# Performance work log

Measured on AMD Instinct MI355X. Metric: run time of the kernel, lower is better.

## Reference

```python
import jax, jax.numpy as jnp
import numpy as np

N = 100000
E = 1600000
F_IN = 256
F_OUT = 128
ALPHA = 0.2  # leaky relu slope


def setup_inputs() -> dict:
    key = jax.random.key(0)
    ks = jax.random.split(key, 8)
    x = jax.random.normal(ks[0], (N, F_IN), dtype=jnp.float32)
    edge_index = jax.random.randint(ks[1], (2, E), 0, N, dtype=jnp.int64)
    edge_attr = jax.random.normal(ks[2], (E,), dtype=jnp.float32)
    # xavier-normal-ish params
    weight = jax.random.normal(ks[3], (F_IN, F_OUT), dtype=jnp.float32) * (1.414 * np.sqrt(2.0 / (F_IN + F_OUT)))
    bias = jnp.zeros((F_OUT,), dtype=jnp.float32)
    a_l = jax.random.normal(ks[4], (F_OUT,), dtype=jnp.float32) * 0.1
    a_r = jax.random.normal(ks[5], (F_OUT,), dtype=jnp.float32) * 0.1
    fc = jax.random.normal(ks[6], (F_OUT, 1), dtype=jnp.float32) * (1.414 * np.sqrt(2.0 / (F_OUT + 1)))
    bf = jnp.zeros((1,), dtype=jnp.float32)
    return {"x": x, "edge_index": edge_index, "edge_attr": edge_attr,
            "weight": weight, "bias": bias, "a_l": a_l, "a_r": a_r,
            "fc": fc, "bf": bf}


def _segment_softmax(val, seg, num_segments):
    # numerically stable softmax over edges grouped by destination row
    seg_max = jax.ops.segment_max(val, seg, num_segments=num_segments)
    val = jnp.exp(val - seg_max[seg])
    seg_sum = jax.ops.segment_sum(val, seg, num_segments=num_segments)
    return val / (seg_sum[seg] + 1e-16)


def reference(x, edge_index, edge_attr, weight, bias, a_l, a_r, fc, bf):
    # dropout layers are identity in eval mode (deterministic reference)
    h = x @ weight                                   # [N, F_OUT]
    row, col = edge_index[0], edge_index[1]          # dst, src
    # GAT-style edge attention: leaky_relu(a_l.h[dst] + a_r.h[src])
    score_l = h @ a_l                                # [N]
    score_r = h @ a_r                                # [N]
    e = score_l[row] + score_r[col]                  # [E]
    e = jnp.where(e > 0, e, ALPHA * e)
    # row-softmax normalization over incoming edges of each dst node
    val = _segment_softmax(e, row, N)                # [E]
    # spmm: out[i] = sum_{(i,j) in E} val_ij * h[j]
    val_h = jax.ops.segment_sum(val[:, None] * h[col], row, num_segments=N)  # [N, F_OUT]
    val_h = jnp.where(jnp.isnan(val_h), 0.0, val_h)
    val_h = val_h + bias
    # NodeAdaptiveEncoder: relu(x) + sigmoid(x@fc + bf) * min(x, 0)
    gate = jax.nn.sigmoid(val_h @ fc + bf)           # [N, 1]
    out = jnp.where(val_h < 0, 0.0, val_h) + gate * jnp.where(val_h > 0, 0.0, val_h)
    return out
```

## Files before the change

### kernel.cpp

```cpp
#include <hip/hip_runtime.h>

#define N_NODES 100000
#define N_EDGES 1600000
#define FIN 256
#define FOUT 128
#define LRELU_ALPHA 0.2f
#define LOG2E 1.4426950408889634f

#define NBUCKET 391
#define PBLOCKS 256
#define PCHUNK  (N_EDGES / PBLOCKS)
#define BCAP    5120

using bf16x8 = __attribute__((ext_vector_type(8))) short;
using f32x4  = __attribute__((ext_vector_type(4))) float;

static __device__ __forceinline__ unsigned short f2bf(float f) {
    union { float f; unsigned u; } v; v.f = f;
    unsigned r = (v.u + 0x7FFF + ((v.u >> 16) & 1)) >> 16;
    return (unsigned short)r;
}

static __device__ __forceinline__ bf16x8 cvt8(float4 a, float4 b) {
    union { bf16x8 v; unsigned short u[8]; } r;
    r.u[0] = f2bf(a.x); r.u[1] = f2bf(a.y); r.u[2] = f2bf(a.z); r.u[3] = f2bf(a.w);
    r.u[4] = f2bf(b.x); r.u[5] = f2bf(b.y); r.u[6] = f2bf(b.z); r.u[7] = f2bf(b.w);
    return r.v;
}

static __device__ __forceinline__ void gld_lds16(const unsigned short* g, unsigned short* l) {
    __builtin_amdgcn_global_load_lds(
        (const __attribute__((address_space(1))) unsigned int*)g,
        (__attribute__((address_space(3))) unsigned int*)l, 16, 0, 0);
}

static __device__ __forceinline__ void acc8(float* acc, uint4 r, float w) {
    union { uint4 u; _Float16 h[8]; } c; c.u = r;
#pragma unroll
    for (int k = 0; k < 8; ++k)
        acc[k] = fmaf((float)c.h[k], w, acc[k]);
}

static __device__ __forceinline__ float edgew(float sl, float sr) {
    float e = sl + sr;
    return exp2f(fmaf(fminf(e, 0.f), LRELU_ALPHA, fmaxf(e, 0.f)));
}

__global__ void k_wt(const float* __restrict__ w, unsigned short* __restrict__ wt_sw,
                     int* __restrict__ bcnt)
{
    if (blockIdx.x == 0)
        for (int z = threadIdx.x; z < NBUCKET; z += 256) bcnt[z] = 0;
    int i = blockIdx.x * blockDim.x + threadIdx.x;
    if (i >= FIN * FOUT) return;
    int k = i >> 7, n = i & 127;
    wt_sw[n * FIN + (((k >> 3) ^ (n & 7)) << 3) + (k & 7)] = f2bf(w[k * FOUT + n]);
}

__global__ __launch_bounds__(256, 2) void k_gemm3(
    const float* __restrict__ x, const unsigned short* __restrict__ wt_sw,
    const float* __restrict__ a_l, const float* __restrict__ a_r,
    unsigned short* __restrict__ hb, float* __restrict__ score_l,
    float* __restrict__ score_r)
{
    __shared__ unsigned short wlds[FOUT * FIN];

    const int tid  = threadIdx.x;
    const int lane = tid & 63;
    const int wid  = tid >> 6;
    const int m    = lane & 15;
    const int q    = lane >> 4;

    {
        const unsigned short* g = wt_sw + wid * 8192;
        unsigned short*       l = wlds  + wid * 8192;
#pragma unroll
        for (int i = 0; i < 16; ++i)
            gld_lds16(g + i * 512 + lane * 8, l + i * 512);
    }

    const int row0 = blockIdx.x * 128 + wid * 32;
    int r0 = row0 + m;       if (r0 > N_NODES - 1) r0 = N_NODES - 1;
    int r1 = row0 + 16 + m;  if (r1 > N_NODES - 1) r1 = N_NODES - 1;
    const float* xp0 = x + (long)r0 * FIN + q * 8;
    const float* xp1 = x + (long)r1 * FIN + q * 8;

    float4 xb[2][2][2];
    xb[0][0][0] = *(const float4*)(xp0);        xb[0][0][1] = *(const float4*)(xp0 + 4);
    xb[0][1][0] = *(const float4*)(xp1);        xb[0][1][1] = *(const float4*)(xp1 + 4);
    xb[1][0][0] = *(const float4*)(xp0 + 32);   xb[1][0][1] = *(const float4*)(xp0 + 36);
    xb[1][1][0] = *(const float4*)(xp1 + 32);   xb[1][1][1] = *(const float4*)(xp1 + 36);

    f32x4 acc[2][8];
#pragma unroll
    for (int mt = 0; mt < 2; ++mt)
#pragma unroll
        for (int nt = 0; nt < 8; ++nt) acc[mt][nt] = (f32x4){0.f, 0.f, 0.f, 0.f};

    __syncthreads();

    const int xr = m & 7;

    bf16x8 bfr[2][8];
#pragma unroll
    for (int nt = 0; nt < 8; ++nt)
        bfr[0][nt] = *(const bf16x8*)&wlds[(nt * 16 + m) * FIN + ((q ^ xr) << 3)];

#pragma unroll
    for (int s = 0; s < 8; ++s) {
        const int p = s & 1;
        bf16x8 a0 = cvt8(xb[p][0][0], xb[p][0][1]);
        bf16x8 a1 = cvt8(xb[p][1][0], xb[p][1][1]);
        if (s + 2 < 8) {
            xb[p][0][0] = *(const float4*)(xp0 + (s + 2) * 32);
            xb[p][0][1] = *(const float4*)(xp0 + (s + 2) * 32 + 4);
            xb[p][1][0] = *(const float4*)(xp1 + (s + 2) * 32);
            xb[p][1][1] = *(const float4*)(xp1 + (s + 2) * 32 + 4);
        }
        if (s + 1 < 8) {
#pragma unroll
            for (int nt = 0; nt < 8; ++nt)
                bfr[1 - p][nt] = *(const bf16x8*)
                    &wlds[(nt * 16 + m) * FIN + ((((s + 1) * 4 + q) ^ xr) << 3)];
        }
#pragma unroll
        for (int nt = 0; nt < 8; ++nt) {
            acc[0][nt] = __builtin_amdgcn_mfma_f32_16x16x32_bf16(bfr[p][nt], a0, acc[0][nt], 0, 0, 0);
            acc[1][nt] = __builtin_amdgcn_mfma_f32_16x16x32_bf16(bfr[p][nt], a1, acc[1][nt], 0, 0, 0);
        }
    }

    _Float16* hh = (_Float16*)hb;

#pragma unroll
    for (int mt = 0; mt < 2; ++mt) {
        const int node = row0 + mt * 16 + m;
        const bool ok = node < N_NODES;
        float sl = 0.f, sr = 0.f;
#pragma unroll
        for (int nt = 0; nt < 8; ++nt) {
            float4 alv = *(const float4*)(a_l + nt * 16 + q * 4);
            float4 arv = *(const float4*)(a_r + nt * 16 + q * 4);
            union { _Float16 h[4]; uint2 u; } pk;
#pragma unroll
            for (int r = 0; r < 4; ++r) {
                float v = acc[mt][nt][r];
                pk.h[r] = (_Float16)v;
                sl = fmaf(v, (&alv.x)[r], sl);
                sr = fmaf(v, (&arv.x)[r], sr);
            }
            if (ok) *(uint2*)&hh[node * FOUT + nt * 16 + q * 4] = pk.u;
        }
        sl += __shfl_xor(sl, 16, 64); sl += __shfl_xor(sl, 32, 64);
        sr += __shfl_xor(sr, 16, 64); sr += __shfl_xor(sr, 32, 64);
        if (ok && q == 0) {
            score_l[node] = sl * LOG2E;
            score_r[node] = sr * LOG2E;
        }
    }
}

__global__ __launch_bounds__(512) void k_part(const int* __restrict__ ei,
                                              int* __restrict__ bcnt,
                                              unsigned* __restrict__ part)
{
    __shared__ unsigned staging[PCHUNK];
    __shared__ unsigned short bkt[PCHUNK];
    __shared__ int cnt[512];
    __shared__ int loc[512];
    __shared__ int gbase[NBUCKET];

    const int tid = threadIdx.x;
    const int e0  = blockIdx.x * PCHUNK;

    cnt[tid] = 0;
    __syncthreads();

    for (int i = tid; i < PCHUNK; i += 512)
        atomicAdd(&cnt[ei[e0 + i] >> 8], 1);
    __syncthreads();

    int v = cnt[tid];
    loc[tid] = v;
    __syncthreads();
    for (int off = 1; off < 512; off <<= 1) {
        int t = (tid >= off) ? loc[tid - off] : 0;
        __syncthreads();
        loc[tid] += t;
        __syncthreads();
    }
    int excl = loc[tid] - v;
    if (tid < NBUCKET && v > 0) gbase[tid] = atomicAdd(&bcnt[tid], v);
    loc[tid] = excl;
    cnt[tid] = excl;
    __syncthreads();

    for (int i = tid; i < PCHUNK; i += 512) {
        int dst = ei[e0 + i];
        int src = ei[N_EDGES + e0 + i];
        int b = dst >> 8;
        unsigned rec = ((unsigned)(dst & 255) << 17) | (unsigned)src;
        int p = atomicAdd(&cnt[b], 1);
        staging[p] = rec;
        bkt[p] = (unsigned short)b;
    }
    __syncthreads();

    for (int i = tid; i < PCHUNK; i += 512) {
        int b = bkt[i];
        int off = gbase[b] + (i - loc[b]);
        if (off < BCAP) part[b * BCAP + off] = staging[i];
    }
}

__global__ __launch_bounds__(512) void k_bucket(const unsigned* __restrict__ part,
                                                const int* __restrict__ bcnt,
                                                int* __restrict__ rowbeg,
                                                int* __restrict__ rowend,
                                                unsigned* __restrict__ csrs)
{
    __shared__ unsigned rin[BCAP];
    __shared__ unsigned rs[BCAP];
    __shared__ int hist[256];
    __shared__ int tmp[512];

    const int b   = blockIdx.x;
    const int tid = threadIdx.x;
    const int beg = b * BCAP;
    int cnt = bcnt[b];
    if (cnt > BCAP) cnt = BCAP;
    const int d0 = b << 8;

    if (tid < 256) hist[tid] = 0;
    __syncthreads();

    for (int i = tid; i < cnt; i += 512) {
        unsigned rec = part[beg + i];
        rin[i] = rec;
        atomicAdd(&hist[rec >> 17], 1);
    }
    __syncthreads();

    int v = (tid < 256) ? hist[tid] : 0;
    tmp[tid] = v;
    __syncthreads();
    for (int off = 1; off < 512; off <<= 1) {
        int t = (tid >= off) ? tmp[tid - off] : 0;
        __syncthreads();
        tmp[tid] += t;
        __syncthreads();
    }
    if (tid < 256) {
        int excl = tmp[tid] - v;
        hist[tid] = excl;
        int d = d0 + tid;
        if (d < N_NODES) { rowbeg[d] = beg + excl; rowend[d] = beg + excl + v; }
    }
    __syncthreads();

    for (int i = tid; i < cnt; i += 512) {
        unsigned rec = rin[i];
        int p = atomicAdd(&hist[rec >> 17], 1);
        rs[p] = rec;
    }
    __syncthreads();

    for (int i = tid; i < cnt; i += 512)
        csrs[beg + i] = rs[i];
}

__global__ __launch_bounds__(256) void k_spmm_gate(
    const int* __restrict__ rowbeg, const int* __restrict__ rowend,
    const unsigned* __restrict__ csrs,
    const unsigned short* __restrict__ hb,
    const float* __restrict__ score_l, const float* __restrict__ score_r,
    const float* __restrict__ bias, const float* __restrict__ fc,
    const float* __restrict__ bf, float* __restrict__ out, int node0)
{
    const int lane = threadIdx.x & 63;
    const int g    = lane >> 4;
    const int t    = lane & 15;
    const int node = node0 + blockIdx.x * 4 + (threadIdx.x >> 6);
    if (node >= N_NODES) return;

    const int beg = rowbeg[node], end = rowend[node];
    const float sl = score_l[node];
    const unsigned short* __restrict__ hq = hb + (t << 3);

    float acc[8] = {0.f, 0.f, 0.f, 0.f, 0.f, 0.f, 0.f, 0.f};
    float denom = 0.f;

    if (end > beg) {
        const int nit  = (end - beg + 3) >> 2;
        const int nv   = nit - 1;
        const int last = end - 1;
        int j = beg + g;

        unsigned rec1;
        float sr0; uint4 r0;
        {
            unsigned rec0 = csrs[min(j, last)];
            rec1 = csrs[min(j + 4, last)];
            int s0 = rec0 & 0x1FFFF;
            sr0 = score_r[s0];
            r0  = *(const uint4*)(hq + (s0 << 7));
        }

        int i = 0;
        for (; i + 2 <= nv; i += 2) {
            unsigned rec2 = csrs[min(j + 8, last)];
            int s1 = rec1 & 0x1FFFF;
            float sr1 = score_r[s1];
            uint4 r1  = *(const uint4*)(hq + (s1 << 7));
            float w0 = edgew(sl, sr0);
            denom += w0;
            acc8(acc, r0, w0);
            j += 4;
            unsigned rec3 = csrs[min(j + 8, last)];
            int s2 = rec2 & 0x1FFFF;
            float sr2 = score_r[s2];
            uint4 r2  = *(const uint4*)(hq + (s2 << 7));
            float w1 = edgew(sl, sr1);
            denom += w1;
            acc8(acc, r1, w1);
            j += 4;
            rec1 = rec3; sr0 = sr2; r0 = r2;
        }
        if (i < nv) {
            int s1 = rec1 & 0x1FFFF;
            float sr1 = score_r[s1];
            uint4 r1  = *(const uint4*)(hq + (s1 << 7));
            float w0 = edgew(sl, sr0);
            denom += w0;
            acc8(acc, r0, w0);
            j += 4;
            sr0 = sr1; r0 = r1;
        }
        {
            float w = (j < end) ? edgew(sl, sr0) : 0.f;
            denom += w;
            acc8(acc, r0, w);
        }
    }

#pragma unroll
    for (int k = 0; k < 8; ++k) {
        acc[k] += __shfl_xor(acc[k], 16, 64);
        acc[k] += __shfl_xor(acc[k], 32, 64);
    }
    denom += __shfl_xor(denom, 16, 64);
    denom += __shfl_xor(denom, 32, 64);

    const float inv = 1.0f / (denom + 1e-16f);

    float vx[8];
    float gp = 0.f;
#pragma unroll
    for (int i = 0; i < 8; ++i) {
        vx[i] = fmaf(acc[i], inv, bias[t * 8 + i]);
        gp = fmaf(vx[i], fc[t * 8 + i], gp);
    }
#pragma unroll
    for (int msk = 1; msk < 16; msk <<= 1) gp += __shfl_xor(gp, msk, 64);
    const float gate = 1.0f / (1.0f + __expf(-(gp + bf[0])));

    float4 o;
    float* ov = &o.x;
    if (g == 0) {
#pragma unroll
        for (int i = 0; i < 4; ++i) {
            float v2 = vx[i];
            ov[i] = (v2 < 0.f ? 0.f : v2) + gate * (v2 > 0.f ? 0.f : v2);
        }
        *(float4*)&out[node * FOUT + t * 8] = o;
    } else if (g == 1) {
#pragma unroll
        for (int i = 0; i < 4; ++i) {
            float v2 = vx[4 + i];
            ov[i] = (v2 < 0.f ? 0.f : v2) + gate * (v2 > 0.f ? 0.f : v2);
        }
        *(float4*)&out[node * FOUT + t * 8 + 4] = o;
    }
}

extern "C" void kernel_launch(void* const* d_in, const int* in_sizes, int n_in,
                              void* d_out, int out_size, void* d_ws, size_t ws_size,
                              hipStream_t stream)
{
    const float* x      = (const float*)d_in[0];
    const int*   ei     = (const int*)d_in[1];
    const float* weight = (const float*)d_in[3];
    const float* bias   = (const float*)d_in[4];
    const float* a_l    = (const float*)d_in[5];
    const float* a_r    = (const float*)d_in[6];
    const float* fc     = (const float*)d_in[7];
    const float* bf     = (const float*)d_in[8];
    float* out = (float*)d_out;

    char* ws = (char*)d_ws;
    unsigned short* hb      = (unsigned short*)(ws);
    unsigned short* wt_sw   = (unsigned short*)(ws + 25600000);
    float*          score_l = (float*)(ws + 25665536);
    float*          score_r = (float*)(ws + 26065536);
    int*            bcnt    = (int*)  (ws + 26465536);
    int*            rowbeg  = (int*)  (ws + 26467584);
    int*            rowend  = (int*)  (ws + 26867584);
    unsigned*       part    = (unsigned*)(ws + 27267584);
    unsigned*       csrs    = (unsigned*)(ws + 35275264);

    k_wt<<<(FIN * FOUT + 255) / 256, 256, 0, stream>>>(weight, wt_sw, bcnt);

    k_gemm3<<<(N_NODES + 127) / 128, 256, 0, stream>>>(
        x, wt_sw, a_l, a_r, hb, score_l, score_r);

    k_part<<<PBLOCKS, 512, 0, stream>>>(ei, bcnt, part);
    k_bucket<<<NBUCKET, 512, 0, stream>>>(part, bcnt, rowbeg, rowend, csrs);

    k_spmm_gate<<<12500, 256, 0, stream>>>(
        rowbeg, rowend, csrs, hb, score_l, score_r, bias, fc, bf, out, 0);
    k_spmm_gate<<<12500, 256, 0, stream>>>(
        rowbeg, rowend, csrs, hb, score_l, score_r, bias, fc, bf, out, 50000);
}
```

Baseline: 296.9 us.

## Replace two-level bucket sort CSR build with atomic histogram, scan and scatter

Swaps the LDS-based two-pass bucket partition (k_part/k_bucket) for a classic CSR build: a global atomic degree histogram, a three-kernel prefix scan, and an atomic-cursor scatter of source indices. This removes the capped bucket buffer and packed records but adds many global atomics with poor locality and more kernel launches. It also merges the two spmm launches into one and drops the record unpacking mask. The edge order within each row becomes nondeterministic, which can change the float summation order.

Measured after the change: 461.1 us. +55.3%, slower.

```diff
diff --git a/kernel.cpp b/kernel.cpp
--- a/kernel.cpp
+++ b/kernel.cpp
@@ -8,9 +8,6 @@
 #define LOG2E 1.4426950408889634f
 
 #define NBUCKET 391
-#define PBLOCKS 256
-#define PCHUNK  (N_EDGES / PBLOCKS)
-#define BCAP    5120
 
 using bf16x8 = __attribute__((ext_vector_type(8))) short;
 using f32x4  = __attribute__((ext_vector_type(4))) float;
@@ -47,10 +44,10 @@
 }
 
 __global__ void k_wt(const float* __restrict__ w, unsigned short* __restrict__ wt_sw,
-                     int* __restrict__ bcnt)
-{
-    if (blockIdx.x == 0)
-        for (int z = threadIdx.x; z < NBUCKET; z += 256) bcnt[z] = 0;
+                     int* __restrict__ deg)
+{
+    for (int z = blockIdx.x * 256 + threadIdx.x; z < N_NODES; z += 128 * 256)
+        deg[z] = 0;
     int i = blockIdx.x * blockDim.x + threadIdx.x;
     if (i >= FIN * FOUT) return;
     int k = i >> 7, n = i & 127;
@@ -160,113 +157,86 @@
     }
 }
 
-__global__ __launch_bounds__(512) void k_part(const int* __restrict__ ei,
-                                              int* __restrict__ bcnt,
-                                              unsigned* __restrict__ part)
-{
-    __shared__ unsigned staging[PCHUNK];
-    __shared__ unsigned short bkt[PCHUNK];
-    __shared__ int cnt[512];
-    __shared__ int loc[512];
-    __shared__ int gbase[NBUCKET];
-
+__global__ __launch_bounds__(256) void k_hist(const int* __restrict__ ei,
+                                              int* __restrict__ deg)
+{
+    int i = (blockIdx.x * 256 + threadIdx.x) * 4;
+    if (i >= N_EDGES) return;
+    int4 d4 = *(const int4*)&ei[i];
+    atomicAdd(&deg[d4.x], 1);
+    atomicAdd(&deg[d4.y], 1);
+    atomicAdd(&deg[d4.z], 1);
+    atomicAdd(&deg[d4.w], 1);
+}
+
+__global__ __launch_bounds__(256) void k_scan1(const int* __restrict__ deg,
+                                               int* __restrict__ pexc,
+                                               int* __restrict__ bsum)
+{
+    __shared__ int s[256];
     const int tid = threadIdx.x;
-    const int e0  = blockIdx.x * PCHUNK;
-
-    cnt[tid] = 0;
+    const int d   = (blockIdx.x << 8) + tid;
+    int v = (d < N_NODES) ? deg[d] : 0;
+    s[tid] = v;
     __syncthreads();
-
-    for (int i = tid; i < PCHUNK; i += 512)
-        atomicAdd(&cnt[ei[e0 + i] >> 8], 1);
+    int acc = v;
+    for (int off = 1; off < 256; off <<= 1) {
+        int t = (tid >= off) ? s[tid - off] : 0;
+        __syncthreads();
+        acc += t;
+        s[tid] = acc;
+        __syncthreads();
+    }
+    if (d < N_NODES) pexc[d] = acc - v;
+    if (tid == 255) bsum[blockIdx.x] = acc;
+}
+
+__global__ __launch_bounds__(512) void k_scan2(const int* __restrict__ bsum,
+                                               int* __restrict__ bbase)
+{
+    __shared__ int s[512];
+    const int tid = threadIdx.x;
+    int v = (tid < NBUCKET) ? bsum[tid] : 0;
+    s[tid] = v;
     __syncthreads();
-
-    int v = cnt[tid];
-    loc[tid] = v;
-    __syncthreads();
+    int acc = v;
     for (int off = 1; off < 512; off <<= 1) {
-        int t = (tid >= off) ? loc[tid - off] : 0;
+        int t = (tid >= off) ? s[tid - off] : 0;
         __syncthreads();
-        loc[tid] += t;
+        acc += t;
+        s[tid] = acc;
         __syncthreads();
     }
-    int excl = loc[tid] - v;
-    if (tid < NBUCKET && v > 0) gbase[tid] = atomicAdd(&bcnt[tid], v);
-    loc[tid] = excl;
-    cnt[tid] = excl;
-    __syncthreads();
-
-    for (int i = tid; i < PCHUNK; i += 512) {
-        int dst = ei[e0 + i];
-        int src = ei[N_EDGES + e0 + i];
-        int b = dst >> 8;
-        unsigned rec = ((unsigned)(dst & 255) << 17) | (unsigned)src;
-        int p = atomicAdd(&cnt[b], 1);
-        staging[p] = rec;
-        bkt[p] = (unsigned short)b;
-    }
-    __syncthreads();
-
-    for (int i = tid; i < PCHUNK; i += 512) {
-        int b = bkt[i];
-        int off = gbase[b] + (i - loc[b]);
-        if (off < BCAP) part[b * BCAP + off] = staging[i];
-    }
-}
-
-__global__ __launch_bounds__(512) void k_bucket(const unsigned* __restrict__ part,
-                                                const int* __restrict__ bcnt,
-                                                int* __restrict__ rowbeg,
-                                                int* __restrict__ rowend,
-                                                unsigned* __restrict__ csrs)
-{
-    __shared__ unsigned rin[BCAP];
-    __shared__ unsigned rs[BCAP];
-    __shared__ int hist[256];
-    __shared__ int tmp[512];
-
-    const int b   = blockIdx.x;
-    const int tid = threadIdx.x;
-    const int beg = b * BCAP;
-    int cnt = bcnt[b];
-    if (cnt > BCAP) cnt = BCAP;
-    const int d0 = b << 8;
-
-    if (tid < 256) hist[tid] = 0;
-    __syncthreads();
-
-    for (int i = tid; i < cnt; i += 512) {
-        unsigned rec = part[beg + i];
-        rin[i] = rec;
-        atomicAdd(&hist[rec >> 17], 1);
-    }
-    __syncthreads();
-
-    int v = (tid < 256) ? hist[tid] : 0;
-    tmp[tid] = v;
-    __syncthreads();
-    for (int off = 1; off < 512; off <<= 1) {
-        int t = (tid >= off) ? tmp[tid - off] : 0;
-        __syncthreads();
-        tmp[tid] += t;
-        __syncthreads();
-    }
-    if (tid < 256) {
-        int excl = tmp[tid] - v;
-        hist[tid] = excl;
-        int d = d0 + tid;
-        if (d < N_NODES) { rowbeg[d] = beg + excl; rowend[d] = beg + excl + v; }
-    }
-    __syncthreads();
-
-    for (int i = tid; i < cnt; i += 512) {
-        unsigned rec = rin[i];
-        int p = atomicAdd(&hist[rec >> 17], 1);
-        rs[p] = rec;
-    }
-    __syncthreads();
-
-    for (int i = tid; i < cnt; i += 512)
-        csrs[beg + i] = rs[i];
+    if (tid < NBUCKET) bbase[tid] = acc - v;
+}
+
+__global__ __launch_bounds__(256) void k_scan3(const int* __restrict__ deg,
+                                               const int* __restrict__ pexc,
+                                               const int* __restrict__ bbase,
+                                               int* __restrict__ rowbeg,
+                                               int* __restrict__ rowend,
+                                               int* __restrict__ cur)
+{
+    const int d = (blockIdx.x << 8) + threadIdx.x;
+    if (d >= N_NODES) return;
+    int rb = bbase[blockIdx.x] + pexc[d];
+    rowbeg[d] = rb;
+    rowend[d] = rb + deg[d];
+    cur[d]    = rb;
+}
+
+__global__ __launch_bounds__(256) void k_scatter(const int* __restrict__ ei,
+                                                 int* __restrict__ cur,
+                                                 unsigned* __restrict__ csrs)
+{
+    int i = (blockIdx.x * 256 + threadIdx.x) * 4;
+    if (i >= N_EDGES) return;
+    int4 d4 = *(const int4*)&ei[i];
+    int4 s4 = *(const int4*)&ei[N_EDGES + i];
+    int p0 = atomicAdd(&cur[d4.x], 1); csrs[p0] = (unsigned)s4.x;
+    int p1 = atomicAdd(&cur[d4.y], 1); csrs[p1] = (unsigned)s4.y;
+    int p2 = atomicAdd(&cur[d4.z], 1); csrs[p2] = (unsigned)s4.z;
+    int p3 = atomicAdd(&cur[d4.w], 1); csrs[p3] = (unsigned)s4.w;
 }
 
 __global__ __launch_bounds__(256) void k_spmm_gate(
@@ -275,12 +245,12 @@
     const unsigned short* __restrict__ hb,
     const float* __restrict__ score_l, const float* __restrict__ score_r,
     const float* __restrict__ bias, const float* __restrict__ fc,
-    const float* __restrict__ bf, float* __restrict__ out, int node0)
+    const float* __restrict__ bf, float* __restrict__ out)
 {
     const int lane = threadIdx.x & 63;
     const int g    = lane >> 4;
     const int t    = lane & 15;
-    const int node = node0 + blockIdx.x * 4 + (threadIdx.x >> 6);
+    const int node = blockIdx.x * 4 + (threadIdx.x >> 6);
     if (node >= N_NODES) return;
 
     const int beg = rowbeg[node], end = rowend[node];
@@ -296,40 +266,36 @@
         const int last = end - 1;
         int j = beg + g;
 
-        unsigned rec1;
+        int s1n;
         float sr0; uint4 r0;
         {
-            unsigned rec0 = csrs[min(j, last)];
-            rec1 = csrs[min(j + 4, last)];
-            int s0 = rec0 & 0x1FFFF;
+            int s0 = (int)csrs[min(j, last)];
+            s1n    = (int)csrs[min(j + 4, last)];
             sr0 = score_r[s0];
             r0  = *(const uint4*)(hq + (s0 << 7));
         }
 
         int i = 0;
         for (; i + 2 <= nv; i += 2) {
-            unsigned rec2 = csrs[min(j + 8, last)];
-            int s1 = rec1 & 0x1FFFF;
-            float sr1 = score_r[s1];
-            uint4 r1  = *(const uint4*)(hq + (s1 << 7));
+            int s2n = (int)csrs[min(j + 8, last)];
+            float sr1 = score_r[s1n];
+            uint4 r1  = *(const uint4*)(hq + (s1n << 7));
             float w0 = edgew(sl, sr0);
             denom += w0;
             acc8(acc, r0, w0);
             j += 4;
-            unsigned rec3 = csrs[min(j + 8, last)];
-            int s2 = rec2 & 0x1FFFF;
-            float sr2 = score_r[s2];
-            uint4 r2  = *(const uint4*)(hq + (s2 << 7));
+            int s3n = (int)csrs[min(j + 8, last)];
+            float sr2 = score_r[s2n];
+            uint4 r2  = *(const uint4*)(hq + (s2n << 7));
             float w1 = edgew(sl, sr1);
             denom += w1;
             acc8(acc, r1, w1);
             j += 4;
-            rec1 = rec3; sr0 = sr2; r0 = r2;
+            s1n = s3n; sr0 = sr2; r0 = r2;
         }
         if (i < nv) {
-            int s1 = rec1 & 0x1FFFF;
-            float sr1 = score_r[s1];
-            uint4 r1  = *(const uint4*)(hq + (s1 << 7));
+            float sr1 = score_r[s1n];
+            uint4 r1  = *(const uint4*)(hq + (s1n << 7));
             float w0 = edgew(sl, sr0);
             denom += w0;
             acc8(acc, r0, w0);
@@ -402,22 +368,26 @@
     unsigned short* wt_sw   = (unsigned short*)(ws + 25600000);
     float*          score_l = (float*)(ws + 25665536);
     float*          score_r = (float*)(ws + 26065536);
-    int*            bcnt    = (int*)  (ws + 26465536);
-    int*            rowbeg  = (int*)  (ws + 26467584);
-    int*            rowend  = (int*)  (ws + 26867584);
-    unsigned*       part    = (unsigned*)(ws + 27267584);
-    unsigned*       csrs    = (unsigned*)(ws + 35275264);
-
-    k_wt<<<(FIN * FOUT + 255) / 256, 256, 0, stream>>>(weight, wt_sw, bcnt);
+    int*            deg     = (int*)  (ws + 26465536);
+    int*            pexc    = (int*)  (ws + 26865536);
+    int*            rowbeg  = (int*)  (ws + 27265536);
+    int*            rowend  = (int*)  (ws + 27665536);
+    int*            cur     = (int*)  (ws + 28065536);
+    int*            bsum    = (int*)  (ws + 28465536);
+    int*            bbase   = (int*)  (ws + 28467584);
+    unsigned*       csrs    = (unsigned*)(ws + 28469632);
+
+    k_wt<<<(FIN * FOUT + 255) / 256, 256, 0, stream>>>(weight, wt_sw, deg);
+
+    k_hist<<<(N_EDGES / 4 + 255) / 256, 256, 0, stream>>>(ei, deg);
+    k_scan1<<<NBUCKET, 256, 0, stream>>>(deg, pexc, bsum);
+    k_scan2<<<1, 512, 0, stream>>>(bsum, bbase);
+    k_scan3<<<NBUCKET, 256, 0, stream>>>(deg, pexc, bbase, rowbeg, rowend, cur);
+    k_scatter<<<(N_EDGES / 4 + 255) / 256, 256, 0, stream>>>(ei, cur, csrs);
 
     k_gemm3<<<(N_NODES + 127) / 128, 256, 0, stream>>>(
         x, wt_sw, a_l, a_r, hb, score_l, score_r);
 
-    k_part<<<PBLOCKS, 512, 0, stream>>>(ei, bcnt, part);
-    k_bucket<<<NBUCKET, 512, 0, stream>>>(part, bcnt, rowbeg, rowend, csrs);
-
-    k_spmm_gate<<<12500, 256, 0, stream>>>(
-        rowbeg, rowend, csrs, hb, score_l, score_r, bias, fc, bf, out, 0);
-    k_spmm_gate<<<12500, 256, 0, stream>>>(
-        rowbeg, rowend, csrs, hb, score_l, score_r, bias, fc, bf, out, 50000);
-}
+    k_spmm_gate<<<(N_NODES + 3) / 4, 256, 0, stream>>>(
+        rowbeg, rowend, csrs, hb, score_l, score_r, bias, fc, bf, out);
+}
```
